# Kernel tuning notes

Measured on AMD Instinct MI355X. Metric: run time of the kernel, lower is better.

Reference implementation:

```python
import jax, jax.numpy as jnp
import numpy as np
import math

NUM_HEADS = 16


def build_hier_idx(seq_len):
    """Vectorized port of build_hierarchical_index_lookup_table.
    Returns [seq_len, log2(seq_len)] int32 neighbor indices into the
    concatenated [leaves | internal nodes] array of length 2*seq_len-1.
    For power-of-two seq_len every entry is valid (no -1s)."""
    assert seq_len & (seq_len - 1) == 0
    level_num = int(math.log2(seq_len))
    cur = np.arange(seq_len, dtype=np.int64)
    cols = []
    for lvl in range(level_num):
        if lvl == 0:
            nxt = cur ^ 1
        else:
            nxt = (cur // 2 + seq_len) ^ 1  # python precedence: (cur//2 + seq_len) ^ 1
        cols.append(nxt)
        cur = nxt
    return np.stack(cols, axis=1)  # [seq_len, level_num]


def setup_inputs() -> dict:
    key = jax.random.key(0)
    ks = jax.random.split(key, 9)
    B, N, D = 2, 2048, 1024
    s = 1.0 / math.sqrt(D)
    return {
        "query": jax.random.normal(ks[0], (B, N, D), jnp.float32),
        "key": jax.random.normal(ks[1], (B, N, D), jnp.float32),
        "value": jax.random.normal(ks[2], (B, N, D), jnp.float32),
        "y": jax.random.normal(ks[3], (B, N - 1, D), jnp.float32),
        "Wq": jax.random.normal(ks[4], (D, D), jnp.float32) * s,
        "Wk": jax.random.normal(ks[5], (D, D), jnp.float32) * s,
        "Wv": jax.random.normal(ks[6], (D, D), jnp.float32) * s,
        "Wo": jax.random.normal(ks[7], (D, D), jnp.float32) * s,
        "bo": jax.random.normal(ks[8], (D,), jnp.float32) * 0.01,
    }


def reference(query, key, value, y, Wq, Wk, Wv, Wo, bo):
    # Sparse path: L_Q == L_K == L_V and y is not None -> update_X_from_Y + out_proj_x.
    # key/value are unused in this branch (only their lengths are checked).
    B, N, D = query.shape
    H = NUM_HEADS
    Dh = D // H
    scale = 1.0 / math.sqrt(Dh)

    idx = jnp.asarray(build_hier_idx(N))          # [N, Lv], Lv = log2(N)

    xy = jnp.concatenate([query, y], axis=1)      # [B, 2N-1, D]
    Q = (query @ Wq.T).reshape(B, N, H, Dh).transpose(0, 2, 1, 3)   # [B,H,N,Dh]
    Kf = (xy @ Wk.T).reshape(B, -1, H, Dh).transpose(0, 2, 1, 3)    # [B,H,2N-1,Dh]
    Vf = (xy @ Wv.T).reshape(B, -1, H, Dh).transpose(0, 2, 1, 3)

    K_self = Kf[:, :, :N, :]                      # [B,H,N,Dh]
    V_self = Vf[:, :, :N, :]
    Kn = Kf[:, :, idx, :]                         # [B,H,N,Lv,Dh] gather over tree levels
    Vn = Vf[:, :, idx, :]

    self_logits = jnp.einsum('bhnd,bhnd->bhn', Q, K_self) * scale          # [B,H,N]
    nbr_logits = jnp.einsum('bhnd,bhnld->bhnl', Q, Kn) * scale             # [B,H,N,Lv]

    all_logits = jnp.concatenate([self_logits[..., None], nbr_logits], axis=-1)  # [B,H,N,1+Lv]
    all_v = jnp.concatenate([V_self[:, :, :, None, :], Vn], axis=3)              # [B,H,N,1+Lv,Dh]

    w = jax.nn.softmax(all_logits, axis=-1)
    out = jnp.einsum('bhnl,bhnld->bhnd', w, all_v)                               # [B,H,N,Dh]
    out = out.transpose(0, 2, 1, 3).reshape(B, N, D)
    return out @ Wo.T + bo
```

## Files before the change

kernel.cpp:

```cpp
#include <hip/hip_runtime.h>
#include <hip/hip_bf16.h>
#include <cstdint>
#include <cstddef>

#define B_ 2
#define N_ 2048
#define D_ 1024
#define H_ 16
#define DH_ 64
#define XYROWS 4095
#define NL 12

typedef __attribute__((ext_vector_type(8))) short bf16x8;
typedef __attribute__((ext_vector_type(4))) float f32x4;

__device__ __forceinline__ float bf2f(unsigned short u) {
    union { unsigned int i; float f; } v; v.i = ((unsigned int)u) << 16; return v.f;
}
__device__ __forceinline__ float asf(unsigned int u) {
    union { unsigned int i; float f; } v; v.i = u; return v.f;
}
__device__ __forceinline__ unsigned short f2bf(float f) {
    union { float f; unsigned int i; } v; v.f = f;
    unsigned int u = v.i;
    unsigned int r = u + 0x7FFFu + ((u >> 16) & 1u);
    return (unsigned short)(r >> 16);
}

__device__ __forceinline__ void ld8(const unsigned short* p, float* o) {
    uint4 u = *(const uint4*)p;
    o[0] = asf(u.x << 16); o[1] = asf(u.x & 0xffff0000u);
    o[2] = asf(u.y << 16); o[3] = asf(u.y & 0xffff0000u);
    o[4] = asf(u.z << 16); o[5] = asf(u.z & 0xffff0000u);
    o[6] = asf(u.w << 16); o[7] = asf(u.w & 0xffff0000u);
}

__global__ void cvt_bf16(const float* __restrict__ src,
                         unsigned short* __restrict__ dst, int nchunks) {
    int c = blockIdx.x * blockDim.x + threadIdx.x;
    if (c >= nchunks) return;
    size_t i = (size_t)c * 8;
    float4 a = *(const float4*)(src + i);
    float4 b = *(const float4*)(src + i + 4);
    union { unsigned short us[8]; uint4 u4; } o;
    o.us[0] = f2bf(a.x); o.us[1] = f2bf(a.y); o.us[2] = f2bf(a.z); o.us[3] = f2bf(a.w);
    o.us[4] = f2bf(b.x); o.us[5] = f2bf(b.y); o.us[6] = f2bf(b.z); o.us[7] = f2bf(b.w);
    *(uint4*)(dst + i) = o.u4;
}

__global__ void build_xy(const float* __restrict__ q, const float* __restrict__ y,
                         unsigned short* __restrict__ xy) {
    int c = blockIdx.x * blockDim.x + threadIdx.x;
    int total = B_ * XYROWS * (D_ / 8);
    if (c >= total) return;
    int col8 = (c & (D_ / 8 - 1)) * 8;
    int rg = c >> 7;
    int b = (rg >= XYROWS) ? 1 : 0;
    int r = rg - b * XYROWS;
    const float* src;
    if (r < N_) src = q + ((size_t)b * N_ + r) * D_ + col8;
    else        src = y + ((size_t)b * (N_ - 1) + (r - N_)) * D_ + col8;
    float4 a = *(const float4*)(src);
    float4 bb = *(const float4*)(src + 4);
    union { unsigned short us[8]; uint4 u4; } o;
    o.us[0] = f2bf(a.x);  o.us[1] = f2bf(a.y);  o.us[2] = f2bf(a.z);  o.us[3] = f2bf(a.w);
    o.us[4] = f2bf(bb.x); o.us[5] = f2bf(bb.y); o.us[6] = f2bf(bb.z); o.us[7] = f2bf(bb.w);
    *(uint4*)(xy + (size_t)rg * D_ + col8) = o.u4;
}

template<bool OUTF32, bool BIAS>
__global__ __launch_bounds__(256, 2)
void gemm_bt(const unsigned short* __restrict__ A, const unsigned short* __restrict__ W,
             void* __restrict__ Cv, const float* __restrict__ bias, int M,
             size_t strideA, size_t strideC) {
    constexpr int K = 1024, Nn = 1024;
    constexpr int BK = 64, LDSS = 72;
    __shared__ __align__(16) unsigned short la[128 * LDSS];
    __shared__ __align__(16) unsigned short lb[128 * LDSS];

    const unsigned short* Ab = A + (size_t)blockIdx.z * strideA;
    int tid = threadIdx.x;
    int row0 = blockIdx.x * 128;
    int col0 = blockIdx.y * 128;
    int wave = tid >> 6, lane = tid & 63;
    int wm = wave >> 1, wn = wave & 1;
    int q4 = lane >> 4, r = lane & 15;

    f32x4 acc[4][4];
    f32x4 zero = {0.f, 0.f, 0.f, 0.f};
#pragma unroll
    for (int i = 0; i < 4; i++)
#pragma unroll
        for (int j = 0; j < 4; j++) acc[i][j] = zero;

    for (int k0 = 0; k0 < K; k0 += BK) {
#pragma unroll
        for (int p = 0; p < 4; p++) {
            int slot = p * 256 + tid;
            int row = slot >> 3;
            int c8 = (slot & 7) * 8;
            int ar = row0 + row; if (ar >= M) ar = M - 1;
            uint4 va = *(const uint4*)(Ab + (size_t)ar * K + k0 + c8);
            uint4 vb = *(const uint4*)(W + (size_t)(col0 + row) * K + k0 + c8);
            *(uint4*)(&la[row * LDSS + c8]) = va;
            *(uint4*)(&lb[row * LDSS + c8]) = vb;
        }
        __syncthreads();
#pragma unroll
        for (int ks = 0; ks < 2; ks++) {
            bf16x8 af[4], bfv[4];
#pragma unroll
            for (int i = 0; i < 4; i++)
                af[i] = *(const bf16x8*)(&la[(wm * 64 + i * 16 + r) * LDSS + ks * 32 + q4 * 8]);
#pragma unroll
            for (int j = 0; j < 4; j++)
                bfv[j] = *(const bf16x8*)(&lb[(wn * 64 + j * 16 + r) * LDSS + ks * 32 + q4 * 8]);
#pragma unroll
            for (int i = 0; i < 4; i++)
#pragma unroll
                for (int j = 0; j < 4; j++)
                    acc[i][j] = __builtin_amdgcn_mfma_f32_16x16x32_bf16(af[i], bfv[j], acc[i][j], 0, 0, 0);
        }
        __syncthreads();
    }

    float bv[4];
    if (BIAS) {
#pragma unroll
        for (int j = 0; j < 4; j++) bv[j] = bias[col0 + wn * 64 + j * 16 + r];
    }
#pragma unroll
    for (int i = 0; i < 4; i++) {
#pragma unroll
        for (int j = 0; j < 4; j++) {
            int col = col0 + wn * 64 + j * 16 + r;
#pragma unroll
            for (int reg = 0; reg < 4; reg++) {
                int row = row0 + wm * 64 + i * 16 + q4 * 4 + reg;
                if (row < M) {
                    float v = acc[i][j][reg];
                    if (BIAS) v += bv[j];
                    if (OUTF32)
                        ((float*)Cv)[(size_t)blockIdx.z * strideC + (size_t)row * Nn + col] = v;
                    else
                        ((unsigned short*)Cv)[(size_t)blockIdx.z * strideC + (size_t)row * Nn + col] = f2bf(v);
                }
            }
        }
    }
}

__global__ __launch_bounds__(256)
void attn_kernel(const unsigned short* __restrict__ Q, const unsigned short* __restrict__ K,
                 const unsigned short* __restrict__ V, unsigned short* __restrict__ O) {
    int t = threadIdx.x;
    int half = t >> 7;
    int c = t & 127;
    int b = blockIdx.y;
    int n = blockIdx.x * 2 + half;

    int rows[NL];
    rows[0] = n;
    int cur = n ^ 1;
    rows[1] = cur;
#pragma unroll
    for (int l = 1; l < 11; l++) {
        cur = ((cur >> 1) + N_) ^ 1;
        rows[l + 1] = cur;
    }

    const unsigned short* Kb = K + (size_t)b * XYROWS * D_;
    const unsigned short* Vb = V + (size_t)b * XYROWS * D_;
    size_t qoff = ((size_t)b * N_ + n) * D_ + (size_t)c * 8;

    float q[8];
    ld8(Q + qoff, q);

    float logits[NL];
#pragma unroll
    for (int j = 0; j < NL; j++) {
        float kv[8];
        ld8(Kb + (size_t)rows[j] * D_ + (size_t)c * 8, kv);
        float p = 0.f;
#pragma unroll
        for (int e = 0; e < 8; e++) p = fmaf(q[e], kv[e], p);
        p += __shfl_xor(p, 1);
        p += __shfl_xor(p, 2);
        p += __shfl_xor(p, 4);
        logits[j] = p * 0.125f;
    }

    float mx = logits[0];
#pragma unroll
    for (int j = 1; j < NL; j++) mx = fmaxf(mx, logits[j]);
    float s = 0.f, w[NL];
#pragma unroll
    for (int j = 0; j < NL; j++) { w[j] = __expf(logits[j] - mx); s += w[j]; }
    float inv = 1.f / s;

    float acc[8] = {0.f, 0.f, 0.f, 0.f, 0.f, 0.f, 0.f, 0.f};
#pragma unroll
    for (int j = 0; j < NL; j++) {
        float vv[8];
        ld8(Vb + (size_t)rows[j] * D_ + (size_t)c * 8, vv);
        float wj = w[j] * inv;
#pragma unroll
        for (int e = 0; e < 8; e++) acc[e] = fmaf(wj, vv[e], acc[e]);
    }

    union { unsigned short us[8]; uint4 u4; } o;
#pragma unroll
    for (int e = 0; e < 8; e++) o.us[e] = f2bf(acc[e]);
    *(uint4*)(O + qoff) = o.u4;
}

extern "C" void kernel_launch(void* const* d_in, const int* in_sizes, int n_in,
                              void* d_out, int out_size, void* d_ws, size_t ws_size,
                              hipStream_t stream) {
    const float* query = (const float*)d_in[0];
    const float* y  = (const float*)d_in[3];
    const float* Wq = (const float*)d_in[4];
    const float* Wk = (const float*)d_in[5];
    const float* Wv = (const float*)d_in[6];
    const float* Wo = (const float*)d_in[7];
    const float* bo = (const float*)d_in[8];
    float* out = (float*)d_out;

    char* ws = (char*)d_ws;
    size_t off = 0;
    auto alloc = [&](size_t bytes) {
        void* p = ws + off; off += (bytes + 255) & ~(size_t)255; return p;
    };
    unsigned short* xy  = (unsigned short*)alloc((size_t)B_ * XYROWS * D_ * 2);
    unsigned short* wqb = (unsigned short*)alloc((size_t)D_ * D_ * 2);
    unsigned short* wkb = (unsigned short*)alloc((size_t)D_ * D_ * 2);
    unsigned short* wvb = (unsigned short*)alloc((size_t)D_ * D_ * 2);
    unsigned short* wob = (unsigned short*)alloc((size_t)D_ * D_ * 2);
    unsigned short* Qb  = (unsigned short*)alloc((size_t)B_ * N_ * D_ * 2);
    unsigned short* Kb  = (unsigned short*)alloc((size_t)B_ * XYROWS * D_ * 2);
    unsigned short* Vb  = (unsigned short*)alloc((size_t)B_ * XYROWS * D_ * 2);
    unsigned short* At  = (unsigned short*)alloc((size_t)B_ * N_ * D_ * 2);

    {
        int total = B_ * XYROWS * (D_ / 8);
        build_xy<<<(total + 255) / 256, 256, 0, stream>>>(query, y, xy);
        int wch = D_ * D_ / 8;
        int wblk = (wch + 255) / 256;
        cvt_bf16<<<wblk, 256, 0, stream>>>(Wq, wqb, wch);
        cvt_bf16<<<wblk, 256, 0, stream>>>(Wk, wkb, wch);
        cvt_bf16<<<wblk, 256, 0, stream>>>(Wv, wvb, wch);
        cvt_bf16<<<wblk, 256, 0, stream>>>(Wo, wob, wch);
    }

    {
        dim3 g(N_ / 128, 8, B_);
        gemm_bt<false, false><<<g, 256, 0, stream>>>(
            xy, wqb, Qb, nullptr, N_, (size_t)XYROWS * D_, (size_t)N_ * D_);
    }
    {
        int M = B_ * XYROWS;
        dim3 g((M + 127) / 128, 8, 1);
        gemm_bt<false, false><<<g, 256, 0, stream>>>(xy, wkb, Kb, nullptr, M, 0, 0);
        gemm_bt<false, false><<<g, 256, 0, stream>>>(xy, wvb, Vb, nullptr, M, 0, 0);
    }
    {
        dim3 g(N_ / 2, B_);
        attn_kernel<<<g, 256, 0, stream>>>(Qb, Kb, Vb, At);
    }
    {
        dim3 g((B_ * N_) / 128, 8, 1);
        gemm_bt<true, true><<<g, 256, 0, stream>>>(At, wob, out, bo, B_ * N_, 0, 0);
    }
}
```

Before: 248.3 us.

## Fuse QKV projections into one GEMM and load tiles via global_load_lds

Concatenates Wq/Wk/Wv into one 3072-wide weight and runs a single GEMM over all xy rows, so attention reads Q, K and V from one interleaved buffer. The four weight conversions become one launch. The GEMM tile loads switch from register round-trips to direct global-to-LDS loads with an unpadded layout. Q is now also computed for the y rows, which adds some wasted work, and the unpadded LDS layout may cause bank conflicts on the fragment reads.

```diff
diff --git a/kernel.cpp b/kernel.cpp
--- a/kernel.cpp
+++ b/kernel.cpp
@@ -10,13 +10,11 @@
 #define DH_ 64
 #define XYROWS 4095
 #define NL 12
+#define QKVN 3072
 
 typedef __attribute__((ext_vector_type(8))) short bf16x8;
 typedef __attribute__((ext_vector_type(4))) float f32x4;
 
-__device__ __forceinline__ float bf2f(unsigned short u) {
-    union { unsigned int i; float f; } v; v.i = ((unsigned int)u) << 16; return v.f;
-}
 __device__ __forceinline__ float asf(unsigned int u) {
     union { unsigned int i; float f; } v; v.i = u; return v.f;
 }
@@ -35,11 +33,22 @@
     o[6] = asf(u.w << 16); o[7] = asf(u.w & 0xffff0000u);
 }
 
-__global__ void cvt_bf16(const float* __restrict__ src,
-                         unsigned short* __restrict__ dst, int nchunks) {
+__device__ __forceinline__ void gload_lds16(const unsigned short* g, unsigned short* l) {
+    __builtin_amdgcn_global_load_lds(
+        (const __attribute__((address_space(1))) unsigned int*)g,
+        (__attribute__((address_space(3))) unsigned int*)l,
+        16, 0, 0);
+}
+
+__global__ void cvt_weights(const float* __restrict__ Wq, const float* __restrict__ Wk,
+                            const float* __restrict__ Wv, const float* __restrict__ Wo,
+                            unsigned short* __restrict__ wqkv, unsigned short* __restrict__ wob) {
     int c = blockIdx.x * blockDim.x + threadIdx.x;
-    if (c >= nchunks) return;
-    size_t i = (size_t)c * 8;
+    int which = c >> 17;
+    int idx = c & 131071;
+    const float* src = (which == 0) ? Wq : (which == 1) ? Wk : (which == 2) ? Wv : Wo;
+    unsigned short* dst = (which < 3) ? (wqkv + (size_t)which * D_ * D_) : wob;
+    size_t i = (size_t)idx * 8;
     float4 a = *(const float4*)(src + i);
     float4 b = *(const float4*)(src + i + 4);
     union { unsigned short us[8]; uint4 u4; } o;
@@ -71,14 +80,11 @@
 template<bool OUTF32, bool BIAS>
 __global__ __launch_bounds__(256, 2)
 void gemm_bt(const unsigned short* __restrict__ A, const unsigned short* __restrict__ W,
-             void* __restrict__ Cv, const float* __restrict__ bias, int M,
-             size_t strideA, size_t strideC) {
-    constexpr int K = 1024, Nn = 1024;
-    constexpr int BK = 64, LDSS = 72;
-    __shared__ __align__(16) unsigned short la[128 * LDSS];
-    __shared__ __align__(16) unsigned short lb[128 * LDSS];
-
-    const unsigned short* Ab = A + (size_t)blockIdx.z * strideA;
+             void* __restrict__ Cv, const float* __restrict__ bias, int M, int Nn) {
+    constexpr int K = 1024, BK = 64;
+    __shared__ __align__(16) unsigned short la[128 * 64];
+    __shared__ __align__(16) unsigned short lb[128 * 64];
+
     int tid = threadIdx.x;
     int row0 = blockIdx.x * 128;
     int col0 = blockIdx.y * 128;
@@ -86,6 +92,9 @@
     int wm = wave >> 1, wn = wave & 1;
     int q4 = lane >> 4, r = lane & 15;
 
+    int rseg = lane >> 3;
+    int cseg = (lane & 7) * 8;
+
     f32x4 acc[4][4];
     f32x4 zero = {0.f, 0.f, 0.f, 0.f};
 #pragma unroll
@@ -96,14 +105,11 @@
     for (int k0 = 0; k0 < K; k0 += BK) {
 #pragma unroll
         for (int p = 0; p < 4; p++) {
-            int slot = p * 256 + tid;
-            int row = slot >> 3;
-            int c8 = (slot & 7) * 8;
-            int ar = row0 + row; if (ar >= M) ar = M - 1;
-            uint4 va = *(const uint4*)(Ab + (size_t)ar * K + k0 + c8);
-            uint4 vb = *(const uint4*)(W + (size_t)(col0 + row) * K + k0 + c8);
-            *(uint4*)(&la[row * LDSS + c8]) = va;
-            *(uint4*)(&lb[row * LDSS + c8]) = vb;
+            int seg = wave * 4 + p;
+            int rloc = seg * 8 + rseg;
+            int ar = row0 + rloc; if (ar >= M) ar = M - 1;
+            gload_lds16(A + (size_t)ar * K + k0 + cseg, &la[seg * 512]);
+            gload_lds16(W + (size_t)(col0 + rloc) * K + k0 + cseg, &lb[seg * 512]);
         }
         __syncthreads();
 #pragma unroll
@@ -111,10 +117,10 @@
             bf16x8 af[4], bfv[4];
 #pragma unroll
             for (int i = 0; i < 4; i++)
-                af[i] = *(const bf16x8*)(&la[(wm * 64 + i * 16 + r) * LDSS + ks * 32 + q4 * 8]);
+                af[i] = *(const bf16x8*)(&la[(wm * 64 + i * 16 + r) * 64 + ks * 32 + q4 * 8]);
 #pragma unroll
             for (int j = 0; j < 4; j++)
-                bfv[j] = *(const bf16x8*)(&lb[(wn * 64 + j * 16 + r) * LDSS + ks * 32 + q4 * 8]);
+                bfv[j] = *(const bf16x8*)(&lb[(wn * 64 + j * 16 + r) * 64 + ks * 32 + q4 * 8]);
 #pragma unroll
             for (int i = 0; i < 4; i++)
 #pragma unroll
@@ -141,9 +147,9 @@
                     float v = acc[i][j][reg];
                     if (BIAS) v += bv[j];
                     if (OUTF32)
-                        ((float*)Cv)[(size_t)blockIdx.z * strideC + (size_t)row * Nn + col] = v;
+                        ((float*)Cv)[(size_t)row * Nn + col] = v;
                     else
-                        ((unsigned short*)Cv)[(size_t)blockIdx.z * strideC + (size_t)row * Nn + col] = f2bf(v);
+                        ((unsigned short*)Cv)[(size_t)row * Nn + col] = f2bf(v);
                 }
             }
         }
@@ -151,8 +157,7 @@
 }
 
 __global__ __launch_bounds__(256)
-void attn_kernel(const unsigned short* __restrict__ Q, const unsigned short* __restrict__ K,
-                 const unsigned short* __restrict__ V, unsigned short* __restrict__ O) {
+void attn_kernel(const unsigned short* __restrict__ QKV, unsigned short* __restrict__ O) {
     int t = threadIdx.x;
     int half = t >> 7;
     int c = t & 127;
@@ -169,18 +174,17 @@
         rows[l + 1] = cur;
     }
 
-    const unsigned short* Kb = K + (size_t)b * XYROWS * D_;
-    const unsigned short* Vb = V + (size_t)b * XYROWS * D_;
-    size_t qoff = ((size_t)b * N_ + n) * D_ + (size_t)c * 8;
+    const unsigned short* base = QKV + (size_t)b * XYROWS * QKVN;
+    size_t c8 = (size_t)c * 8;
 
     float q[8];
-    ld8(Q + qoff, q);
+    ld8(base + (size_t)n * QKVN + c8, q);
 
     float logits[NL];
 #pragma unroll
     for (int j = 0; j < NL; j++) {
         float kv[8];
-        ld8(Kb + (size_t)rows[j] * D_ + (size_t)c * 8, kv);
+        ld8(base + (size_t)rows[j] * QKVN + D_ + c8, kv);
         float p = 0.f;
 #pragma unroll
         for (int e = 0; e < 8; e++) p = fmaf(q[e], kv[e], p);
@@ -202,7 +206,7 @@
 #pragma unroll
     for (int j = 0; j < NL; j++) {
         float vv[8];
-        ld8(Vb + (size_t)rows[j] * D_ + (size_t)c * 8, vv);
+        ld8(base + (size_t)rows[j] * QKVN + 2 * D_ + c8, vv);
         float wj = w[j] * inv;
 #pragma unroll
         for (int e = 0; e < 8; e++) acc[e] = fmaf(wj, vv[e], acc[e]);
@@ -211,7 +215,7 @@
     union { unsigned short us[8]; uint4 u4; } o;
 #pragma unroll
     for (int e = 0; e < 8; e++) o.us[e] = f2bf(acc[e]);
-    *(uint4*)(O + qoff) = o.u4;
+    *(uint4*)(O + ((size_t)b * N_ + n) * D_ + c8) = o.u4;
 }
 
 extern "C" void kernel_launch(void* const* d_in, const int* in_sizes, int n_in,
@@ -231,44 +235,28 @@
     auto alloc = [&](size_t bytes) {
         void* p = ws + off; off += (bytes + 255) & ~(size_t)255; return p;
     };
-    unsigned short* xy  = (unsigned short*)alloc((size_t)B_ * XYROWS * D_ * 2);
-    unsigned short* wqb = (unsigned short*)alloc((size_t)D_ * D_ * 2);
-    unsigned short* wkb = (unsigned short*)alloc((size_t)D_ * D_ * 2);
-    unsigned short* wvb = (unsigned short*)alloc((size_t)D_ * D_ * 2);
-    unsigned short* wob = (unsigned short*)alloc((size_t)D_ * D_ * 2);
-    unsigned short* Qb  = (unsigned short*)alloc((size_t)B_ * N_ * D_ * 2);
-    unsigned short* Kb  = (unsigned short*)alloc((size_t)B_ * XYROWS * D_ * 2);
-    unsigned short* Vb  = (unsigned short*)alloc((size_t)B_ * XYROWS * D_ * 2);
-    unsigned short* At  = (unsigned short*)alloc((size_t)B_ * N_ * D_ * 2);
+    unsigned short* xy   = (unsigned short*)alloc((size_t)B_ * XYROWS * D_ * 2 + 4096);
+    unsigned short* wqkv = (unsigned short*)alloc((size_t)QKVN * D_ * 2);
+    unsigned short* wob  = (unsigned short*)alloc((size_t)D_ * D_ * 2);
+    unsigned short* QKV  = (unsigned short*)alloc((size_t)B_ * XYROWS * QKVN * 2);
+    unsigned short* At   = (unsigned short*)alloc((size_t)B_ * N_ * D_ * 2);
 
     {
         int total = B_ * XYROWS * (D_ / 8);
         build_xy<<<(total + 255) / 256, 256, 0, stream>>>(query, y, xy);
-        int wch = D_ * D_ / 8;
-        int wblk = (wch + 255) / 256;
-        cvt_bf16<<<wblk, 256, 0, stream>>>(Wq, wqb, wch);
-        cvt_bf16<<<wblk, 256, 0, stream>>>(Wk, wkb, wch);
-        cvt_bf16<<<wblk, 256, 0, stream>>>(Wv, wvb, wch);
-        cvt_bf16<<<wblk, 256, 0, stream>>>(Wo, wob, wch);
-    }
-
-    {
-        dim3 g(N_ / 128, 8, B_);
+        cvt_weights<<<2048, 256, 0, stream>>>(Wq, Wk, Wv, Wo, wqkv, wob);
+    }
+    {
+        dim3 g((B_ * XYROWS + 127) / 128, QKVN / 128);
         gemm_bt<false, false><<<g, 256, 0, stream>>>(
-            xy, wqb, Qb, nullptr, N_, (size_t)XYROWS * D_, (size_t)N_ * D_);
-    }
-    {
-        int M = B_ * XYROWS;
-        dim3 g((M + 127) / 128, 8, 1);
-        gemm_bt<false, false><<<g, 256, 0, stream>>>(xy, wkb, Kb, nullptr, M, 0, 0);
-        gemm_bt<false, false><<<g, 256, 0, stream>>>(xy, wvb, Vb, nullptr, M, 0, 0);
+            xy, wqkv, QKV, nullptr, B_ * XYROWS, QKVN);
     }
     {
         dim3 g(N_ / 2, B_);
-        attn_kernel<<<g, 256, 0, stream>>>(Qb, Kb, Vb, At);
-    }
-    {
-        dim3 g((B_ * N_) / 128, 8, 1);
-        gemm_bt<true, true><<<g, 256, 0, stream>>>(At, wob, out, bo, B_ * N_, 0, 0);
-    }
-}
+        attn_kernel<<<g, 256, 0, stream>>>(QKV, At);
+    }
+    {
+        dim3 g((B_ * N_) / 128, D_ / 128);
+        gemm_bt<true, true><<<g, 256, 0, stream>>>(At, wob, out, bo, B_ * N_, D_);
+    }
+}
```

Result: faster. 228.3 us (-8.1%).
